# Performance work log

Hardware: AMD Instinct MI355X
Metric: run time of the kernel (lower is better)

## Reference

```python
import jax, jax.numpy as jnp
import numpy as np

B, S, D, H, DK, DV = 4, 1024, 1024, 16, 64, 64
EPS = 1e-6


def _cv_layernorm(xr, xi, g_rr, g_ri, g_ii, b_r, b_i):
    # complex layernorm via 2x2 covariance whitening (Deep Complex Networks style)
    mr = xr.mean(-1, keepdims=True)
    mi = xi.mean(-1, keepdims=True)
    r = xr - mr
    i = xi - mi
    Vrr = (r * r).mean(-1, keepdims=True) + EPS
    Vii = (i * i).mean(-1, keepdims=True) + EPS
    Vri = (r * i).mean(-1, keepdims=True)
    s = jnp.sqrt(Vrr * Vii - Vri * Vri)        # sqrt(det V)
    t = jnp.sqrt(Vrr + Vii + 2.0 * s)
    inv = 1.0 / (s * t)
    Wrr = (Vii + s) * inv
    Wii = (Vrr + s) * inv
    Wri = -Vri * inv
    or_ = Wrr * r + Wri * i
    oi = Wri * r + Wii * i
    return g_rr * or_ + g_ri * oi + b_r, g_ri * or_ + g_ii * oi + b_i


def _forward(q_r, q_i, k_r, k_i, v_r, v_i, wq_r, wq_i, wk_r, wk_i, wv_r, wv_i,
             fc_r, fc_i, gamma_rr, gamma_ri, gamma_ii, beta_r, beta_i):
    qc_in = (q_r + 1j * q_i).astype(jnp.complex64)
    kc = (k_r + 1j * k_i).astype(jnp.complex64)
    vc = (v_r + 1j * v_i).astype(jnp.complex64)
    wq = (wq_r + 1j * wq_i).astype(jnp.complex64)
    wk = (wk_r + 1j * wk_i).astype(jnp.complex64)
    wv = (wv_r + 1j * wv_i).astype(jnp.complex64)
    fc = (fc_r + 1j * fc_i).astype(jnp.complex64)

    # complex QKV projections (torch Linear: y = x @ W.T), split into heads
    q = (qc_in @ wq.T).reshape(B, S, H, DK).transpose(0, 2, 1, 3)  # [B,H,S,DK]
    k = (kc @ wk.T).reshape(B, S, H, DK).transpose(0, 2, 1, 3)
    v = (vc @ wv.T).reshape(B, S, H, DV).transpose(0, 2, 1, 3)

    temp = jnp.float32(DK ** 0.5)
    attn = jnp.einsum('bhqd,bhkd->bhqk', q / temp, k)  # complex [B,H,S,S]

    # MagMinMaxNorm over last dim: min-max normalize magnitude, keep phase
    mag = jnp.abs(attn)
    mn = mag.min(-1, keepdims=True)
    mx = mag.max(-1, keepdims=True)
    scale = (mag - mn) / ((mx - mn) * mag + 1e-12)
    attn = attn * scale

    o = jnp.einsum('bhqk,bhkd->bhqd', attn, v)
    o = o.transpose(0, 2, 1, 3).reshape(B, S, H * DV)  # [B,S,H*DV]
    o = o @ fc.T
    o = o + qc_in  # residual
    out_r, out_i = _cv_layernorm(o.real, o.imag, gamma_rr, gamma_ri, gamma_ii, beta_r, beta_i)
    return jnp.stack([out_r, out_i])  # [2,B,S,D]


def setup_inputs() -> dict:
    key = jax.random.key(0)
    ks = jax.random.split(key, 14)
    rn = lambda k, shape, sc=1.0: jax.random.normal(k, shape, jnp.float32) * sc
    ws = 1.0 / np.sqrt(D)
    return {
        'q_r': rn(ks[0], (B, S, D)), 'q_i': rn(ks[1], (B, S, D)),
        'k_r': rn(ks[2], (B, S, D)), 'k_i': rn(ks[3], (B, S, D)),
        'v_r': rn(ks[4], (B, S, D)), 'v_i': rn(ks[5], (B, S, D)),
        'wq_r': rn(ks[6], (H * DK, D), ws), 'wq_i': rn(ks[7], (H * DK, D), ws),
        'wk_r': rn(ks[8], (H * DK, D), ws), 'wk_i': rn(ks[9], (H * DK, D), ws),
        'wv_r': rn(ks[10], (H * DV, D), ws), 'wv_i': rn(ks[11], (H * DV, D), ws),
        'fc_r': rn(ks[12], (D, H * DV), ws), 'fc_i': rn(ks[13], (D, H * DV), ws),
        'gamma_rr': jnp.ones((D,), jnp.float32), 'gamma_ri': jnp.zeros((D,), jnp.float32),
        'gamma_ii': jnp.ones((D,), jnp.float32),
        'beta_r': jnp.zeros((D,), jnp.float32), 'beta_i': jnp.zeros((D,), jnp.float32),
    }


def reference(q_r, q_i, k_r, k_i, v_r, v_i, wq_r, wq_i, wk_r, wk_i, wv_r, wv_i,
              fc_r, fc_i, gamma_rr, gamma_ri, gamma_ii, beta_r, beta_i):
    return _forward(q_r, q_i, k_r, k_i, v_r, v_i, wq_r, wq_i, wk_r, wk_i, wv_r, wv_i,
                    fc_r, fc_i, gamma_rr, gamma_ri, gamma_ii, beta_r, beta_i)
```

## Files before the change

kernel.cpp:

```cpp
#include <hip/hip_runtime.h>
#include <hip/hip_bf16.h>

#define BB 4
#define SS 1024
#define DD 1024
#define HH 16
#define DKH 64
#define EPS_LN 1e-6f

#define M_ROWS 4096
#define KK 2048

typedef float  floatx4 __attribute__((ext_vector_type(4)));
typedef short  shortx8 __attribute__((ext_vector_type(8)));
#define MFMA16(a, b, c) __builtin_amdgcn_mfma_f32_16x16x32_bf16(a, b, c, 0, 0, 0)

__device__ __forceinline__ unsigned pk2(float lo, float hi) {
    unsigned u;
    asm("v_cvt_pk_bf16_f32 %0, %1, %2" : "=v"(u) : "v"(lo), "v"(hi));
    return u;
}

__device__ __forceinline__ ushort f2b(float x) {
    return (ushort)(pk2(x, x) & 0xffffu);
}

__device__ __forceinline__ shortx8 negf(shortx8 x) {
    shortx8 r;
    #pragma unroll
    for (int i = 0; i < 8; ++i) r[i] = (short)(x[i] ^ (short)0x8000);
    return r;
}

__device__ __forceinline__ shortx8 vswap(shortx8 v) {
    union { shortx8 s; unsigned u[4]; } a, b;
    a.s = v;
    #pragma unroll
    for (int i = 0; i < 4; ++i) {
        const unsigned w = a.u[i];
        b.u[i] = ((w >> 16) | (w << 16)) ^ 0x00008000u;
    }
    return b.s;
}

__device__ __forceinline__ void gl16(const void* g, void* l) {
    __builtin_amdgcn_global_load_lds(
        (const __attribute__((address_space(1))) unsigned int*)g,
        (__attribute__((address_space(3))) unsigned int*)l, 16, 0, 0);
}

__global__ __launch_bounds__(256) void pack_x(
    const float* __restrict__ qr, const float* __restrict__ qi,
    const float* __restrict__ kr, const float* __restrict__ ki,
    const float* __restrict__ vr, const float* __restrict__ vi,
    ushort* __restrict__ Xq, ushort* __restrict__ Xk, ushort* __restrict__ Xv)
{
    const int t = blockIdx.y;
    const float* pr = t == 0 ? qr : t == 1 ? kr : vr;
    const float* pi = t == 0 ? qi : t == 1 ? ki : vi;
    ushort* X = t == 0 ? Xq : t == 1 ? Xk : Xv;
    const int idx = blockIdx.x * 256 + threadIdx.x;
    const int row = idx >> 8, c4 = (idx & 255) * 4;
    float4 a = *(const float4*)(pr + (size_t)row * 1024 + c4);
    float4 b = *(const float4*)(pi + (size_t)row * 1024 + c4);
    ushort4 ua; ua.x = f2b(a.x); ua.y = f2b(a.y); ua.z = f2b(a.z); ua.w = f2b(a.w);
    ushort4 ub; ub.x = f2b(b.x); ub.y = f2b(b.y); ub.z = f2b(b.z); ub.w = f2b(b.w);
    *(ushort4*)(X + (size_t)row * KK + c4)        = ua;
    *(ushort4*)(X + (size_t)row * KK + 1024 + c4) = ub;
}

__global__ __launch_bounds__(256) void pack_w(
    const float* __restrict__ ar, const float* __restrict__ ai,
    const float* __restrict__ br, const float* __restrict__ bi,
    const float* __restrict__ cr, const float* __restrict__ ci,
    const float* __restrict__ dr, const float* __restrict__ di,
    ushort* __restrict__ Bq, ushort* __restrict__ Bk,
    ushort* __restrict__ Bv, ushort* __restrict__ Bf)
{
    const int t = blockIdx.y;
    const float* wr = t == 0 ? ar : t == 1 ? br : t == 2 ? cr : dr;
    const float* wi = t == 0 ? ai : t == 1 ? bi : t == 2 ? ci : di;
    ushort* Bo = t == 0 ? Bq : t == 1 ? Bk : t == 2 ? Bv : Bf;
    const int idx = blockIdx.x * 256 + threadIdx.x;
    const int n = idx >> 8, c4 = (idx & 255) * 4;
    float4 a = *(const float4*)(wr + (size_t)n * 1024 + c4);
    float4 b = *(const float4*)(wi + (size_t)n * 1024 + c4);
    ushort4 ua; ua.x = f2b(a.x);  ua.y = f2b(a.y);  ua.z = f2b(a.z);  ua.w = f2b(a.w);
    ushort4 ub; ub.x = f2b(b.x);  ub.y = f2b(b.y);  ub.z = f2b(b.z);  ub.w = f2b(b.w);
    ushort4 un; un.x = f2b(-b.x); un.y = f2b(-b.y); un.z = f2b(-b.z); un.w = f2b(-b.w);
    *(ushort4*)(Bo + (size_t)n * KK + c4)                 = ua;
    *(ushort4*)(Bo + (size_t)n * KK + 1024 + c4)          = un;
    *(ushort4*)(Bo + (size_t)(1024 + n) * KK + c4)        = ub;
    *(ushort4*)(Bo + (size_t)(1024 + n) * KK + 1024 + c4) = ua;
}

#define BM 128
#define BN 128
#define BK 32

__device__ __forceinline__ void bgemm_body(
    const ushort* __restrict__ A, const ushort* __restrict__ Bm,
    void* __restrict__ out0, void* __restrict__ out1,
    const float* __restrict__ resr, const float* __restrict__ resi,
    float scale, int mode, int bx, int by)
{
    __shared__ __align__(16) ushort As[BM * BK];
    __shared__ __align__(16) ushort Bs[BN * BK];

    const int tid = threadIdx.x;
    const int lane = tid & 63, wave = tid >> 6;
    const int l15 = lane & 15, quad = lane >> 4;
    const int m0 = by * BM, n0 = bx * BN;
    const int wm = (wave & 1) * 64, wn = (wave >> 1) * 64;

    const int id0 = tid, id1 = 256 + tid;
    const ushort* ga0 = A  + (size_t)(m0 + (id0 >> 2)) * KK + (id0 & 3) * 8;
    const ushort* ga1 = A  + (size_t)(m0 + (id1 >> 2)) * KK + (id1 & 3) * 8;
    const ushort* gb0 = Bm + (size_t)(n0 + (id0 >> 2)) * KK + (id0 & 3) * 8;
    const ushort* gb1 = Bm + (size_t)(n0 + (id1 >> 2)) * KK + (id1 & 3) * 8;
    ushort* la0 = &As[id0 * 8];
    ushort* la1 = &As[id1 * 8];
    ushort* lb0 = &Bs[id0 * 8];
    ushort* lb1 = &Bs[id1 * 8];

    floatx4 acc[4][4];
    #pragma unroll
    for (int fm = 0; fm < 4; ++fm)
        #pragma unroll
        for (int fn = 0; fn < 4; ++fn)
            acc[fm][fn] = (floatx4){0.f, 0.f, 0.f, 0.f};

    for (int k0 = 0; k0 < KK; k0 += BK) {
        gl16(ga0 + k0, la0);
        gl16(ga1 + k0, la1);
        gl16(gb0 + k0, lb0);
        gl16(gb1 + k0, lb1);
        __syncthreads();

        shortx8 af[4], bf[4];
        #pragma unroll
        for (int f = 0; f < 4; ++f)
            af[f] = *(const shortx8*)&As[(wm + f * 16 + l15) * BK + quad * 8];
        #pragma unroll
        for (int f = 0; f < 4; ++f)
            bf[f] = *(const shortx8*)&Bs[(wn + f * 16 + l15) * BK + quad * 8];
        #pragma unroll
        for (int fm = 0; fm < 4; ++fm)
            #pragma unroll
            for (int fn = 0; fn < 4; ++fn)
                acc[fm][fn] = MFMA16(af[fm], bf[fn], acc[fm][fn]);
        __syncthreads();
    }

    #pragma unroll
    for (int fm = 0; fm < 4; ++fm) {
        #pragma unroll
        for (int fn = 0; fn < 4; ++fn) {
            #pragma unroll
            for (int r = 0; r < 4; ++r) {
                const int m = m0 + wm + fm * 16 + quad * 4 + r;
                const int n = n0 + wn + fn * 16 + l15;
                const float v = acc[fm][fn][r] * scale;
                const int nn = n & 1023;
                const int hh = nn >> 6;
                const int bb = m >> 10, s = m & 1023;
                if (mode == 0) {
                    const int dk = (n < 1024 ? 0 : 64) + (nn & 63);
                    const int tq = s >> 5, row = s & 31;
                    ushort* Qb = (ushort*)out0 +
                        ((size_t)(bb * HH + hh) * 32 + tq) * 4096;
                    const int off = ((row >> 4) * 4 + (dk >> 5)) * 512 +
                                    ((dk >> 3) & 3) * 128 + (row & 15) * 8 + (dk & 7);
                    Qb[off] = f2b(v);
                } else if (mode == 3) {
                    const int dk = (n < 1024 ? 0 : 64) + (nn & 63);
                    const int t = s >> 6, row = s & 63;
                    ushort* Kb = (ushort*)out0 +
                        ((size_t)(bb * HH + hh) * 16 + t) * 8192;
                    const int off = ((row >> 4) * 4 + (dk >> 5)) * 512 +
                                    ((dk >> 3) & 3) * 128 + (row & 15) * 8 + (dk & 7);
                    Kb[off] = f2b(v);
                } else if (mode == 1) {
                    const int dv = nn & 63;
                    const int c = 2 * s + (n < 1024 ? 0 : 1);
                    ushort* Vb = (ushort*)out0 + (size_t)(bb * HH + hh) * 131072;
                    const int off = (((c >> 7) * 4 + (dv >> 4)) * 4 + ((c >> 5) & 3)) * 512 +
                                    ((c >> 3) & 3) * 128 + (dv & 15) * 8 + (c & 7);
                    Vb[off] = f2b(n < 1024 ? v : -v);
                } else {
                    const size_t off = (size_t)m * 1024 + nn;
                    if (n < 1024) ((float*)out0)[off] = v + resr[off];
                    else          ((float*)out1)[off] = v + resi[off];
                }
            }
        }
    }
}

__global__ __launch_bounds__(256) void bgemm_qk(
    const ushort* __restrict__ Xq, const ushort* __restrict__ Xk,
    const ushort* __restrict__ Bq, const ushort* __restrict__ Bk,
    ushort* __restrict__ qpk, ushort* __restrict__ kpk)
{
    const int z = blockIdx.z;
    bgemm_body(z == 0 ? Xq : Xk, z == 0 ? Bq : Bk,
               z == 0 ? (void*)qpk : (void*)kpk, nullptr, nullptr, nullptr,
               z == 0 ? 0.125f : 1.0f, z == 0 ? 0 : 3, blockIdx.x, blockIdx.y);
}

__global__ __launch_bounds__(256) void bgemm_v(
    const ushort* __restrict__ Xv, const ushort* __restrict__ Bv,
    ushort* __restrict__ Vneg)
{
    bgemm_body(Xv, Bv, (void*)Vneg, nullptr, nullptr, nullptr,
               1.0f, 1, blockIdx.x, blockIdx.y);
}

__global__ __launch_bounds__(256) void bgemm_fc(
    const ushort* __restrict__ A, const ushort* __restrict__ Bm,
    float* __restrict__ fr, float* __restrict__ fi,
    const float* __restrict__ resr, const float* __restrict__ resi)
{
    bgemm_body(A, Bm, fr, fi, resr, resi, 1.0f, 2, blockIdx.x, blockIdx.y);
}

#define SWZ(row, col) (((row) << 5) + ((col) ^ (((row) & 7) << 2)))

__device__ __forceinline__ void loadK(shortx8 (&K)[2][4], const ushort* kfb,
                                      int t, int kt_w) {
    #pragma unroll
    for (int kt2 = 0; kt2 < 2; ++kt2)
        #pragma unroll
        for (int f = 0; f < 4; ++f)
            K[kt2][f] = *(const shortx8*)(kfb + t * 8192 +
                                          ((kt_w * 2 + kt2) * 4 + f) * 512);
}

__device__ __forceinline__ void loadVn(shortx8 (&V)[4], const ushort* vfb,
                                       int t, int wave) {
    #pragma unroll
    for (int f = 0; f < 4; ++f)
        V[f] = *(const shortx8*)(vfb + ((t * 4 + wave) * 4 + f) * 512);
}

#define ATTN_ITER(IT, NX, KC, KN)                                             \
  {                                                                           \
    loadVn(V_, vfb, (IT), wave);                                              \
    const int p_ = (IT) & 1;                                                  \
    unsigned* Ab = Abuf[p_][kt_w];                                            \
    unsigned* Pb = Pbuf[p_][kt_w];                                            \
    floatx4 cr[2], ci[2];                                                     \
    _Pragma("unroll")                                                         \
    for (int kt2 = 0; kt2 < 2; ++kt2) {                                       \
      floatx4 r_ = (floatx4){0.f, 0.f, 0.f, 0.f};                             \
      floatx4 i_ = (floatx4){0.f, 0.f, 0.f, 0.f};                             \
      r_ = MFMA16(Aq0, KC[kt2][0], r_); r_ = MFMA16(Aq1, KC[kt2][1], r_);     \
      r_ = MFMA16(Nq2, KC[kt2][2], r_); r_ = MFMA16(Nq3, KC[kt2][3], r_);     \
      i_ = MFMA16(Aq2, KC[kt2][0], i_); i_ = MFMA16(Aq3, KC[kt2][1], i_);     \
      i_ = MFMA16(Aq0, KC[kt2][2], i_); i_ = MFMA16(Aq1, KC[kt2][3], i_);     \
      cr[kt2] = r_; ci[kt2] = i_;                                             \
    }                                                                         \
    loadK(KN, kfb, (NX), kt_w);                                               \
    _Pragma("unroll")                                                         \
    for (int kt2 = 0; kt2 < 2; ++kt2) {                                       \
      _Pragma("unroll")                                                       \
      for (int r = 0; r < 4; ++r) {                                           \
        const float ar = cr[kt2][r], ai = ci[kt2][r];                         \
        const float s2 = fmaf(ar, ar, ai * ai);                               \
        const float irm = s2 > 0.f ? rsqrtf(s2) : 0.f;                        \
        const float mag = s2 * irm;                                           \
        rmn[r] = fminf(rmn[r], mag);                                          \
        rmx[r] = fmaxf(rmx[r], mag);                                          \
        const int row_ = qt_w * 16 + quad * 4 + r;                            \
        const int w_ = SWZ(row_, kt2 * 16 + l15);                             \
        Ab[w_] = pk2(ar, ai);                                                 \
        Pb[w_] = pk2(ar * irm, ai * irm);                                     \
      }                                                                       \
    }                                                                         \
    asm volatile("s_waitcnt lgkmcnt(0)" ::: "memory");                        \
    __builtin_amdgcn_s_barrier();                                             \
    const shortx8 Vs0 = vswap(V_[0]), Vs1 = vswap(V_[1]);                     \
    const shortx8 Vs2 = vswap(V_[2]), Vs3 = vswap(V_[3]);                     \
    const unsigned* A0 = Abuf[p_][0];                                         \
    const unsigned* A1 = Abuf[p_][1];                                         \
    const unsigned* P0 = Pbuf[p_][0];                                         \
    const unsigned* P1 = Pbuf[p_][1];                                         \
    __builtin_amdgcn_s_setprio(1);                                            \
    _Pragma("unroll")                                                         \
    for (int q2 = 0; q2 < 2; ++q2) {                                          \
      const int row_ = q2 * 16 + l15;                                         \
      const int rb_ = row_ * 32, rm_ = (row_ & 7) << 2;                       \
      const int c0_ = rb_ + ((quad * 4) ^ rm_);                               \
      const int c1_ = rb_ + ((16 + quad * 4) ^ rm_);                          \
      shortx8 Af0 = *(const shortx8*)&A0[c0_];                                \
      shortx8 Af1 = *(const shortx8*)&A0[c1_];                                \
      shortx8 Af2 = *(const shortx8*)&A1[c0_];                                \
      shortx8 Af3 = *(const shortx8*)&A1[c1_];                                \
      shortx8 Pf0 = *(const shortx8*)&P0[c0_];                                \
      shortx8 Pf1 = *(const shortx8*)&P0[c1_];                                \
      shortx8 Pf2 = *(const shortx8*)&P1[c0_];                                \
      shortx8 Pf3 = *(const shortx8*)&P1[c1_];                                \
      acc[q2][0] = MFMA16(Af0, V_[0], acc[q2][0]);                            \
      acc[q2][0] = MFMA16(Af1, V_[1], acc[q2][0]);                            \
      acc[q2][0] = MFMA16(Af2, V_[2], acc[q2][0]);                            \
      acc[q2][0] = MFMA16(Af3, V_[3], acc[q2][0]);                            \
      acc[q2][1] = MFMA16(Af0, Vs0, acc[q2][1]);                              \
      acc[q2][1] = MFMA16(Af1, Vs1, acc[q2][1]);                              \
      acc[q2][1] = MFMA16(Af2, Vs2, acc[q2][1]);                              \
      acc[q2][1] = MFMA16(Af3, Vs3, acc[q2][1]);                              \
      acc[q2][2] = MFMA16(Pf0, V_[0], acc[q2][2]);                            \
      acc[q2][2] = MFMA16(Pf1, V_[1], acc[q2][2]);                            \
      acc[q2][2] = MFMA16(Pf2, V_[2], acc[q2][2]);                            \
      acc[q2][2] = MFMA16(Pf3, V_[3], acc[q2][2]);                            \
      acc[q2][3] = MFMA16(Pf0, Vs0, acc[q2][3]);                              \
      acc[q2][3] = MFMA16(Pf1, Vs1, acc[q2][3]);                              \
      acc[q2][3] = MFMA16(Pf2, Vs2, acc[q2][3]);                              \
      acc[q2][3] = MFMA16(Pf3, Vs3, acc[q2][3]);                              \
    }                                                                         \
    __builtin_amdgcn_s_setprio(0);                                            \
  }

__global__ __launch_bounds__(256) void attn_mfma(
    const ushort* __restrict__ qpk, const ushort* __restrict__ kpk,
    const ushort* __restrict__ vn, ushort* __restrict__ xo)
{
    __shared__ unsigned Abuf[2][2][32 * 32];
    __shared__ unsigned Pbuf[2][2][32 * 32];
    __shared__ unsigned mnb[32], mxb[32];

    const int tid  = threadIdx.x;
    const int wave = tid >> 6, lane = tid & 63;
    const int l15  = lane & 15, quad = lane >> 4;
    const int qt_w = wave & 1, kt_w = wave >> 1;

    const int swz = (blockIdx.x & 7) * 256 + (blockIdx.x >> 3);
    const int qt = swz & 31, hb = swz >> 5;
    const int h = hb & 15, b = hb >> 4;
    const size_t qrow0 = (size_t)b * SS + (size_t)qt * 32;

    if (tid < 32) { mnb[tid] = 0x7f800000u; mxb[tid] = 0u; }

    const ushort* qfb = qpk + ((size_t)(b * HH + h) * 32 + qt) * 4096 + lane * 8;
    shortx8 Aq0 = *(const shortx8*)(qfb + (qt_w * 4 + 0) * 512);
    shortx8 Aq1 = *(const shortx8*)(qfb + (qt_w * 4 + 1) * 512);
    shortx8 Aq2 = *(const shortx8*)(qfb + (qt_w * 4 + 2) * 512);
    shortx8 Aq3 = *(const shortx8*)(qfb + (qt_w * 4 + 3) * 512);
    shortx8 Nq2 = negf(Aq2), Nq3 = negf(Aq3);

    const ushort* kfb = kpk + (size_t)(b * HH + h) * 131072 + lane * 8;
    const ushort* vfb = vn  + (size_t)(b * HH + h) * 131072 + lane * 8;

    floatx4 acc[2][4];
    #pragma unroll
    for (int q2 = 0; q2 < 2; ++q2)
        #pragma unroll
        for (int j = 0; j < 4; ++j)
            acc[q2][j] = (floatx4){0.f, 0.f, 0.f, 0.f};
    float rmn[4] = {1e30f, 1e30f, 1e30f, 1e30f};
    float rmx[4] = {0.f, 0.f, 0.f, 0.f};

    shortx8 KA[2][4], KB[2][4], V_[4];
    loadK(KA, kfb, 0, kt_w);

    for (int it = 0; it < 16; it += 2) {
        ATTN_ITER(it,     it + 1,        KA, KB);
        ATTN_ITER(it + 1, (it + 2) & 15, KB, KA);
    }

    #pragma unroll
    for (int r = 0; r < 4; ++r) {
        float mn = rmn[r], mx = rmx[r];
        #pragma unroll
        for (int o = 1; o < 16; o <<= 1) {
            mn = fminf(mn, __shfl_xor(mn, o));
            mx = fmaxf(mx, __shfl_xor(mx, o));
        }
        if (l15 == 0) {
            const int q = qt_w * 16 + quad * 4 + r;
            atomicMin(&mnb[q], __float_as_uint(mn));
            atomicMax(&mxb[q], __float_as_uint(mx));
        }
    }
    __syncthreads();

    #pragma unroll
    for (int q2 = 0; q2 < 2; ++q2) {
        #pragma unroll
        for (int r = 0; r < 4; ++r) {
            const int q = q2 * 16 + quad * 4 + r;
            const float mn = __uint_as_float(mnb[q]);
            const float mx = __uint_as_float(mxb[q]);
            const float d = mx - mn;
            const float invd = d > 0.f ? 1.f / d : 0.f;
            const float vr_ = (acc[q2][0][r] - mn * acc[q2][2][r]) * invd;
            const float vi_ = (acc[q2][1][r] - mn * acc[q2][3][r]) * invd;
            const size_t row = (qrow0 + q) * KK + h * 64 + wave * 16 + l15;
            xo[row]        = f2b(vr_);
            xo[row + 1024] = f2b(vi_);
        }
    }
}

__global__ __launch_bounds__(256) void ln_kernel(
    const float* __restrict__ xr, const float* __restrict__ xi,
    const float* __restrict__ g_rr, const float* __restrict__ g_ri,
    const float* __restrict__ g_ii,
    const float* __restrict__ b_r, const float* __restrict__ b_i,
    float* __restrict__ out)
{
    const int lane = threadIdx.x & 63;
    const int wave = threadIdx.x >> 6;
    const int row  = blockIdx.x * 4 + wave;
    const float* pr = xr + (size_t)row * DD;
    const float* pi = xi + (size_t)row * DD;

    float r[16], im[16];
    float sr = 0.f, si = 0.f;
    #pragma unroll
    for (int j = 0; j < 16; ++j) {
        r[j]  = pr[lane + 64*j];
        im[j] = pi[lane + 64*j];
        sr += r[j]; si += im[j];
    }
    #pragma unroll
    for (int o = 32; o; o >>= 1) { sr += __shfl_xor(sr, o); si += __shfl_xor(si, o); }
    const float mr = sr * (1.f / DD), mi = si * (1.f / DD);

    float srr = 0.f, sii = 0.f, sri = 0.f;
    #pragma unroll
    for (int j = 0; j < 16; ++j) {
        const float a = r[j] - mr, c = im[j] - mi;
        srr = fmaf(a, a, srr); sii = fmaf(c, c, sii); sri = fmaf(a, c, sri);
    }
    #pragma unroll
    for (int o = 32; o; o >>= 1) {
        srr += __shfl_xor(srr, o); sii += __shfl_xor(sii, o); sri += __shfl_xor(sri, o);
    }
    const float Vrr = srr * (1.f / DD) + EPS_LN;
    const float Vii = sii * (1.f / DD) + EPS_LN;
    const float Vri = sri * (1.f / DD);
    const float s  = sqrtf(Vrr * Vii - Vri * Vri);
    const float t  = sqrtf(Vrr + Vii + 2.f * s);
    const float inv = 1.f / (s * t);
    const float Wrr = (Vii + s) * inv;
    const float Wii = (Vrr + s) * inv;
    const float Wri = -Vri * inv;

    #pragma unroll
    for (int j = 0; j < 16; ++j) {
        const int d = lane + 64*j;
        const float a = r[j] - mr, c = im[j] - mi;
        const float or_ = Wrr * a + Wri * c;
        const float oi_ = Wri * a + Wii * c;
        out[(size_t)row * DD + d] = g_rr[d]*or_ + g_ri[d]*oi_ + b_r[d];
        out[(size_t)(M_ROWS) * DD + (size_t)row * DD + d] = g_ri[d]*or_ + g_ii[d]*oi_ + b_i[d];
    }
}

extern "C" void kernel_launch(void* const* d_in, const int* in_sizes, int n_in,
                              void* d_out, int out_size, void* d_ws, size_t ws_size,
                              hipStream_t stream) {
    const float* q_r  = (const float*)d_in[0];
    const float* q_i  = (const float*)d_in[1];
    const float* k_r  = (const float*)d_in[2];
    const float* k_i  = (const float*)d_in[3];
    const float* v_r  = (const float*)d_in[4];
    const float* v_i  = (const float*)d_in[5];
    const float* wq_r = (const float*)d_in[6];
    const float* wq_i = (const float*)d_in[7];
    const float* wk_r = (const float*)d_in[8];
    const float* wk_i = (const float*)d_in[9];
    const float* wv_r = (const float*)d_in[10];
    const float* wv_i = (const float*)d_in[11];
    const float* fc_r = (const float*)d_in[12];
    const float* fc_i = (const float*)d_in[13];
    const float* g_rr = (const float*)d_in[14];
    const float* g_ri = (const float*)d_in[15];
    const float* g_ii = (const float*)d_in[16];
    const float* b_r  = (const float*)d_in[17];
    const float* b_i  = (const float*)d_in[18];
    float* out = (float*)d_out;

    float* ws = (float*)d_ws;
    const size_t NE = (size_t)M_ROWS * 1024;
    ushort* Xq   = (ushort*)(ws + 0 * NE);
    ushort* Xk   = (ushort*)(ws + 1 * NE);
    ushort* Xv   = (ushort*)(ws + 2 * NE);
    ushort* qpk  = (ushort*)(ws + 3 * NE);
    ushort* kpk  = (ushort*)(ws + 4 * NE);
    ushort* Bq   = (ushort*)(ws + 5 * NE);
    ushort* Bk   = Bq + (size_t)KK * KK;
    ushort* Bv   = (ushort*)(ws + 6 * NE);
    ushort* Bf   = Bv + (size_t)KK * KK;
    ushort* Vneg = (ushort*)(ws + 0 * NE);
    ushort* xo   = (ushort*)(ws + 2 * NE);
    float*  fr   = ws + 3 * NE;
    float*  fi   = ws + 4 * NE;

    pack_x<<<dim3(4096, 3), 256, 0, stream>>>(q_r, q_i, k_r, k_i, v_r, v_i, Xq, Xk, Xv);
    pack_w<<<dim3(1024, 4), 256, 0, stream>>>(wq_r, wq_i, wk_r, wk_i, wv_r, wv_i,
                                              fc_r, fc_i, Bq, Bk, Bv, Bf);

    bgemm_qk<<<dim3(KK / BN, M_ROWS / BM, 2), 256, 0, stream>>>(
        Xq, Xk, Bq, Bk, qpk, kpk);

    bgemm_v<<<dim3(KK / BN, M_ROWS / BM), 256, 0, stream>>>(Xv, Bv, Vneg);

    attn_mfma<<<dim3(2048), 256, 0, stream>>>(qpk, kpk, Vneg, xo);

    bgemm_fc<<<dim3(KK / BN, M_ROWS / BM), 256, 0, stream>>>(xo, Bf, fr, fi, q_r, q_i);

    ln_kernel<<<M_ROWS / 4, 256, 0, stream>>>(fr, fi, g_rr, g_ri, g_ii, b_r, b_i, out);
}
```

Measured before the change: 526.7 us.

## Rework bf16 GEMM into double-buffered 128x256x64 tiles with swizzled LDS

Replaces the single-buffered 128x128x32 GEMM loop with a 2-stage pipeline. The next K tile's global-to-LDS loads are issued while the current tile's MFMAs run, with explicit vmcnt waits and barriers. Tiles grow to 128x256 with BK=64 and 512 threads (8 waves), and LDS uses an XOR swizzle to cut bank conflicts; MFMA sections get raised wave priority. The goal is to hide memory latency and remove the per-step double sync in the projection and fc GEMMs, at the cost of far more LDS per block (96KB) and fewer blocks in the grid.

```diff
diff --git a/kernel.cpp b/kernel.cpp
--- a/kernel.cpp
+++ b/kernel.cpp
@@ -94,9 +94,54 @@
     *(ushort4*)(Bo + (size_t)(1024 + n) * KK + 1024 + c4) = ua;
 }
 
-#define BM 128
-#define BN 128
-#define BK 32
+#define GBM 128
+#define GBN 256
+#define GBK 64
+
+#define GSTAGE(P, KT) do {                                                    \
+    const ushort* ga_ = gA + (KT) * GBK;                                      \
+    const ushort* gb_ = gB + (KT) * GBK;                                      \
+    ushort* la_ = &As[P][st8];                                                \
+    ushort* lb_ = &Bs[P][st8];                                                \
+    gl16(ga_,                la_);                                            \
+    gl16(ga_ + 64 * KK,      la_ + 4096);                                     \
+    gl16(gb_,                lb_);                                            \
+    gl16(gb_ + 64 * KK,      lb_ + 4096);                                     \
+    gl16(gb_ + 128 * KK,     lb_ + 8192);                                     \
+    gl16(gb_ + 192 * KK,     lb_ + 12288);                                    \
+} while (0)
+
+#define GKSTEP(P, VM, DOSTAGE) do {                                           \
+    asm volatile("s_waitcnt vmcnt(" #VM ")" ::: "memory");                    \
+    __builtin_amdgcn_s_barrier();                                             \
+    __builtin_amdgcn_sched_barrier(0);                                        \
+    const ushort* Ap = As[P];                                                 \
+    const ushort* Bp = Bs[P];                                                 \
+    shortx8 a[4][2], b[4][2];                                                 \
+    _Pragma("unroll")                                                         \
+    for (int f = 0; f < 4; ++f) {                                             \
+        const int ra = (wm + f * 16 + l15) * GBK;                             \
+        const int rb = (wn + f * 16 + l15) * GBK;                             \
+        a[f][0] = *(const shortx8*)&Ap[ra + ca0];                             \
+        a[f][1] = *(const shortx8*)&Ap[ra + ca1];                             \
+        b[f][0] = *(const shortx8*)&Bp[rb + ca0];                             \
+        b[f][1] = *(const shortx8*)&Bp[rb + ca1];                             \
+    }                                                                         \
+    __builtin_amdgcn_s_setprio(1);                                            \
+    _Pragma("unroll")                                                         \
+    for (int fm = 0; fm < 4; ++fm)                                            \
+        _Pragma("unroll")                                                     \
+        for (int fn = 0; fn < 4; ++fn) {                                      \
+            acc[fm][fn] = MFMA16(a[fm][0], b[fn][0], acc[fm][fn]);            \
+            acc[fm][fn] = MFMA16(a[fm][1], b[fn][1], acc[fm][fn]);            \
+        }                                                                     \
+    __builtin_amdgcn_s_setprio(0);                                            \
+    asm volatile("s_waitcnt lgkmcnt(0)" ::: "memory");                        \
+    __builtin_amdgcn_sched_barrier(0);                                        \
+    __builtin_amdgcn_s_barrier();                                             \
+    if (DOSTAGE) GSTAGE(P, kt + 2);                                           \
+    ++kt;                                                                     \
+} while (0)
 
 __device__ __forceinline__ void bgemm_body(
     const ushort* __restrict__ A, const ushort* __restrict__ Bm,
@@ -104,24 +149,25 @@
     const float* __restrict__ resr, const float* __restrict__ resi,
     float scale, int mode, int bx, int by)
 {
-    __shared__ __align__(16) ushort As[BM * BK];
-    __shared__ __align__(16) ushort Bs[BN * BK];
-
-    const int tid = threadIdx.x;
-    const int lane = tid & 63, wave = tid >> 6;
+    __shared__ __align__(16) ushort As[2][GBM * GBK];
+    __shared__ __align__(16) ushort Bs[2][GBN * GBK];
+
+    const int t = threadIdx.x;
+    const int lane = t & 63, wave = t >> 6;
     const int l15 = lane & 15, quad = lane >> 4;
-    const int m0 = by * BM, n0 = bx * BN;
-    const int wm = (wave & 1) * 64, wn = (wave >> 1) * 64;
-
-    const int id0 = tid, id1 = 256 + tid;
-    const ushort* ga0 = A  + (size_t)(m0 + (id0 >> 2)) * KK + (id0 & 3) * 8;
-    const ushort* ga1 = A  + (size_t)(m0 + (id1 >> 2)) * KK + (id1 & 3) * 8;
-    const ushort* gb0 = Bm + (size_t)(n0 + (id0 >> 2)) * KK + (id0 & 3) * 8;
-    const ushort* gb1 = Bm + (size_t)(n0 + (id1 >> 2)) * KK + (id1 & 3) * 8;
-    ushort* la0 = &As[id0 * 8];
-    ushort* la1 = &As[id1 * 8];
-    ushort* lb0 = &Bs[id0 * 8];
-    ushort* lb1 = &Bs[id1 * 8];
+    const int wm = (wave >> 2) * 64;
+    const int wn = (wave & 3) * 64;
+    const int m0 = by * GBM, n0 = bx * GBN;
+
+    const int srow = t >> 3;
+    const int schk = (t & 7) ^ (srow & 7);
+    const int st8  = t * 8;
+    const ushort* gA = A  + (size_t)(m0 + srow) * KK + schk * 8;
+    const ushort* gB = Bm + (size_t)(n0 + srow) * KK + schk * 8;
+
+    const int rm  = l15 & 7;
+    const int ca0 = ((quad)     ^ rm) * 8;
+    const int ca1 = ((4 + quad) ^ rm) * 8;
 
     floatx4 acc[4][4];
     #pragma unroll
@@ -130,27 +176,16 @@
         for (int fn = 0; fn < 4; ++fn)
             acc[fm][fn] = (floatx4){0.f, 0.f, 0.f, 0.f};
 
-    for (int k0 = 0; k0 < KK; k0 += BK) {
-        gl16(ga0 + k0, la0);
-        gl16(ga1 + k0, la1);
-        gl16(gb0 + k0, lb0);
-        gl16(gb1 + k0, lb1);
-        __syncthreads();
-
-        shortx8 af[4], bf[4];
-        #pragma unroll
-        for (int f = 0; f < 4; ++f)
-            af[f] = *(const shortx8*)&As[(wm + f * 16 + l15) * BK + quad * 8];
-        #pragma unroll
-        for (int f = 0; f < 4; ++f)
-            bf[f] = *(const shortx8*)&Bs[(wn + f * 16 + l15) * BK + quad * 8];
-        #pragma unroll
-        for (int fm = 0; fm < 4; ++fm)
-            #pragma unroll
-            for (int fn = 0; fn < 4; ++fn)
-                acc[fm][fn] = MFMA16(af[fm], bf[fn], acc[fm][fn]);
-        __syncthreads();
-    }
+    GSTAGE(0, 0);
+    GSTAGE(1, 1);
+
+    int kt = 0;
+    for (int i = 0; i < 15; ++i) {
+        GKSTEP(0, 6, 1);
+        GKSTEP(1, 6, 1);
+    }
+    GKSTEP(0, 6, 0);
+    GKSTEP(1, 0, 0);
 
     #pragma unroll
     for (int fm = 0; fm < 4; ++fm) {
@@ -174,9 +209,9 @@
                     Qb[off] = f2b(v);
                 } else if (mode == 3) {
                     const int dk = (n < 1024 ? 0 : 64) + (nn & 63);
-                    const int t = s >> 6, row = s & 63;
+                    const int tt = s >> 6, row = s & 63;
                     ushort* Kb = (ushort*)out0 +
-                        ((size_t)(bb * HH + hh) * 16 + t) * 8192;
+                        ((size_t)(bb * HH + hh) * 16 + tt) * 8192;
                     const int off = ((row >> 4) * 4 + (dk >> 5)) * 512 +
                                     ((dk >> 3) & 3) * 128 + (row & 15) * 8 + (dk & 7);
                     Kb[off] = f2b(v);
@@ -197,7 +232,7 @@
     }
 }
 
-__global__ __launch_bounds__(256) void bgemm_qk(
+__global__ __launch_bounds__(512) void bgemm_qk(
     const ushort* __restrict__ Xq, const ushort* __restrict__ Xk,
     const ushort* __restrict__ Bq, const ushort* __restrict__ Bk,
     ushort* __restrict__ qpk, ushort* __restrict__ kpk)
@@ -208,7 +243,7 @@
                z == 0 ? 0.125f : 1.0f, z == 0 ? 0 : 3, blockIdx.x, blockIdx.y);
 }
 
-__global__ __launch_bounds__(256) void bgemm_v(
+__global__ __launch_bounds__(512) void bgemm_v(
     const ushort* __restrict__ Xv, const ushort* __restrict__ Bv,
     ushort* __restrict__ Vneg)
 {
@@ -216,7 +251,7 @@
                1.0f, 1, blockIdx.x, blockIdx.y);
 }
 
-__global__ __launch_bounds__(256) void bgemm_fc(
+__global__ __launch_bounds__(512) void bgemm_fc(
     const ushort* __restrict__ A, const ushort* __restrict__ Bm,
     float* __restrict__ fr, float* __restrict__ fi,
     const float* __restrict__ resr, const float* __restrict__ resi)
@@ -501,14 +536,14 @@
     pack_w<<<dim3(1024, 4), 256, 0, stream>>>(wq_r, wq_i, wk_r, wk_i, wv_r, wv_i,
                                               fc_r, fc_i, Bq, Bk, Bv, Bf);
 
-    bgemm_qk<<<dim3(KK / BN, M_ROWS / BM, 2), 256, 0, stream>>>(
+    bgemm_qk<<<dim3(KK / GBN, M_ROWS / GBM, 2), 512, 0, stream>>>(
         Xq, Xk, Bq, Bk, qpk, kpk);
 
-    bgemm_v<<<dim3(KK / BN, M_ROWS / BM), 256, 0, stream>>>(Xv, Bv, Vneg);
+    bgemm_v<<<dim3(KK / GBN, M_ROWS / GBM), 512, 0, stream>>>(Xv, Bv, Vneg);
 
     attn_mfma<<<dim3(2048), 256, 0, stream>>>(qpk, kpk, Vneg, xo);
 
-    bgemm_fc<<<dim3(KK / BN, M_ROWS / BM), 256, 0, stream>>>(xo, Bf, fr, fi, q_r, q_i);
+    bgemm_fc<<<dim3(KK / GBN, M_ROWS / GBM), 512, 0, stream>>>(xo, Bf, fr, fi, q_r, q_i);
 
     ln_kernel<<<M_ROWS / 4, 256, 0, stream>>>(fr, fi, g_rr, g_ri, g_ii, b_r, b_i, out);
 }
```

Result: faster. 509.0 us (-3.4%).
